# Optimization experiments

Hardware: AMD Instinct MI355X
Metric: run time of the kernel (lower is better)

Reference implementation:

```python
import jax, jax.numpy as jnp
import numpy as np

ALPHA = 0.2  # LeakyReLU negative slope
NEG_INF = -9e15


def gat_layer(h_in, adj_mask, W, a, concat):
    """Classic pyGAT dense GraphAttentionLayer (eval mode, dropout=identity).
    h_in: [B, N, Fin], adj_mask: [N, N] bool, W: [Fin, Fout], a: [2*Fout, 1].
    """
    h = jnp.einsum('bnf,fo->bno', h_in, W)          # [B, N, Fout]
    Fo = W.shape[1]
    f1 = h @ a[:Fo, 0]                               # [B, N] scores for source
    f2 = h @ a[Fo:, 0]                               # [B, N] scores for target
    e = jax.nn.leaky_relu(f1[:, :, None] + f2[:, None, :], negative_slope=ALPHA)
    e = jnp.where(adj_mask[None, :, :], e, NEG_INF)  # mask non-edges
    attn = jax.nn.softmax(e, axis=-1)                # normalize over neighbors
    out = jnp.einsum('bij,bjo->bio', attn, h)        # weighted aggregation
    return jax.nn.elu(out) if concat else out


def setup_inputs() -> dict:
    key = jax.random.key(0)
    ks = jax.random.split(key, 7)
    B, T, N = 2, 17, 1024
    nfeat, nhid, nclass, nheads = 64, 64, 64, 4
    x = jax.random.normal(ks[0], (B, T, N, nfeat), dtype=jnp.float32)
    adj = jax.random.randint(ks[1], (N, N), 0, 2, dtype=jnp.int32)
    W_heads = jax.random.normal(ks[2], (nheads, nfeat, nhid), dtype=jnp.float32) / np.sqrt(nfeat)
    a_heads = jax.random.normal(ks[3], (nheads, 2 * nhid, 1), dtype=jnp.float32) / np.sqrt(2 * nhid)
    W_out = jax.random.normal(ks[4], (nhid * nheads, nclass), dtype=jnp.float32) / np.sqrt(nhid * nheads)
    a_out = jax.random.normal(ks[5], (2 * nclass, 1), dtype=jnp.float32) / np.sqrt(2 * nclass)
    return {"x": x, "adj": adj, "W_heads": W_heads, "a_heads": a_heads,
            "W_out": W_out, "a_out": a_out, "pred_step": 1}


def reference(x, adj, W_heads, a_heads, W_out, a_out, pred_step):
    B, T, N, F = x.shape
    Tp = T - pred_step
    mask = adj > 0
    # All time steps are independent -> fold (B, Tp) into one batch axis.
    xt = x[:, :Tp].reshape(B * Tp, N, F)
    nheads = W_heads.shape[0]
    heads = [gat_layer(xt, mask, W_heads[h], a_heads[h], concat=True)
             for h in range(nheads)]
    hcat = jnp.concatenate(heads, axis=-1)           # [B*Tp, N, nhid*nheads]
    out = jax.nn.relu(gat_layer(hcat, mask, W_out, a_out, concat=False))
    return out.reshape(B, Tp, N, -1)
```

## Files before the change

kernel.cpp:

```cpp
#include <hip/hip_runtime.h>
#include <hip/hip_bf16.h>

typedef short bf16x8 __attribute__((ext_vector_type(8)));
typedef float f32x4 __attribute__((ext_vector_type(4)));
typedef _Float16 half8 __attribute__((ext_vector_type(8)));
typedef _Float16 half4 __attribute__((ext_vector_type(4)));
typedef __fp16 cvt2_t __attribute__((ext_vector_type(2)));

#define N_NODES 1024
#define FDIM 64
#define NG 32
#define LOG2E 1.44269504088896f

__global__ __launch_bounds__(256) void k_maskf(const int* __restrict__ adj,
                                               __hip_bfloat16* __restrict__ Madd) {
    int w = blockIdx.x * 256 + threadIdx.x;
    const int* p = adj + (size_t)w * 32;
    union { bf16x8 v[4]; __hip_bfloat16 hh[32]; } u;
#pragma unroll
    for (int b = 0; b < 32; b++)
        u.hh[b] = __float2bfloat16(p[b] > 0 ? 0.f : -2048.f);
    bf16x8* dst = (bf16x8*)(Madd + (size_t)w * 32);
#pragma unroll
    for (int q = 0; q < 4; q++) dst[q] = u.v[q];
}

__global__ __launch_bounds__(256) void k_prepw(const float* __restrict__ Wh,
                                               const float* __restrict__ Wo,
                                               _Float16* __restrict__ wt1,
                                               _Float16* __restrict__ wt2) {
    const int t = threadIdx.x;
    {
        const int h = t >> 6, o = t & 63;
        const float* src = Wh + (size_t)h * 4096 + o;
#pragma unroll
        for (int k0 = 0; k0 < 64; k0 += 8) {
            union { half8 v; cvt2_t c[4]; } pk_;
#pragma unroll
            for (int kk = 0; kk < 8; kk += 2)
                pk_.c[kk >> 1] = __builtin_amdgcn_cvt_pkrtz(src[(k0 + kk) * 64],
                                                            src[(k0 + kk + 1) * 64]);
            *(half8*)(wt1 + (size_t)t * 64 + k0) = pk_.v;
        }
    }
    {
        const int kq = t >> 6, o = t & 63;
        const float* src = Wo + o;
#pragma unroll
        for (int k0 = kq * 64; k0 < kq * 64 + 64; k0 += 8) {
            union { half8 v; cvt2_t c[4]; } pk_;
#pragma unroll
            for (int kk = 0; kk < 8; kk += 2)
                pk_.c[kk >> 1] = __builtin_amdgcn_cvt_pkrtz(src[(k0 + kk) * 64],
                                                            src[(k0 + kk + 1) * 64]);
            *(half8*)(wt2 + (size_t)o * 256 + k0) = pk_.v;
        }
    }
}

__global__ __launch_bounds__(512, 2) void k_proj1(const float* __restrict__ x,
                                                  const _Float16* __restrict__ wt1,
                                                  const float* __restrict__ ah,
                                                  _Float16* __restrict__ H1T,
                                                  float* __restrict__ F1,
                                                  float* __restrict__ F2) {
    __shared__ _Float16 xs[128][64];
    const int t = threadIdx.x;
    const int nb = blockIdx.x, g = blockIdx.y;
    const int n0 = nb * 128;
    const int b = g >> 4, tstep = g & 15;

    {
        const int r = t >> 2, cq = t & 3;
        const float* xr = x + (((size_t)(b * 17 + tstep) * N_NODES + n0 + r) * FDIM) + cq * 16;
        float4 v0 = *(const float4*)(xr);
        float4 v1 = *(const float4*)(xr + 4);
        float4 v2 = *(const float4*)(xr + 8);
        float4 v3 = *(const float4*)(xr + 12);
        union { half8 v; cvt2_t c[4]; } u0, u1;
        u0.c[0] = __builtin_amdgcn_cvt_pkrtz(v0.x, v0.y);
        u0.c[1] = __builtin_amdgcn_cvt_pkrtz(v0.z, v0.w);
        u0.c[2] = __builtin_amdgcn_cvt_pkrtz(v1.x, v1.y);
        u0.c[3] = __builtin_amdgcn_cvt_pkrtz(v1.z, v1.w);
        u1.c[0] = __builtin_amdgcn_cvt_pkrtz(v2.x, v2.y);
        u1.c[1] = __builtin_amdgcn_cvt_pkrtz(v2.z, v2.w);
        u1.c[2] = __builtin_amdgcn_cvt_pkrtz(v3.x, v3.y);
        u1.c[3] = __builtin_amdgcn_cvt_pkrtz(v3.z, v3.w);
        *(half8*)&xs[r][((2 * cq) ^ (r & 7)) * 8] = u0.v;
        *(half8*)&xs[r][((2 * cq + 1) ^ (r & 7)) * 8] = u1.v;
    }
    __syncthreads();

    const int wv = t >> 6, ln = t & 63, li = ln & 15, grp = ln >> 4;
    const int arow = wv * 16 + li;

    f32x4 acc[16];
#pragma unroll
    for (int q = 0; q < 16; q++) acc[q] = (f32x4){0.f, 0.f, 0.f, 0.f};

#pragma unroll
    for (int s = 0; s < 2; s++) {
        half8 af = *(const half8*)&xs[arow][((s * 4 + grp) ^ (arow & 7)) * 8];
#pragma unroll
        for (int tile = 0; tile < 16; tile++) {
            half8 bf = *(const half8*)(wt1 + (size_t)(tile * 16 + li) * 64 + s * 32 + grp * 8);
            acc[tile] = __builtin_amdgcn_mfma_f32_16x16x32_f16(af, bf, acc[tile], 0, 0, 0);
        }
    }

    const int nbase = n0 + wv * 16 + grp * 4;
#pragma unroll
    for (int h = 0; h < 4; h++) {
        float p1[4] = {0.f, 0.f, 0.f, 0.f}, p2[4] = {0.f, 0.f, 0.f, 0.f};
#pragma unroll
        for (int ot = 0; ot < 4; ot++) {
            float a1v = ah[h * 128 + ot * 16 + li];
            float a2v = ah[h * 128 + 64 + ot * 16 + li];
            f32x4 A = acc[h * 4 + ot];
#pragma unroll
            for (int r = 0; r < 4; r++) {
                p1[r] = fmaf(A[r], a1v, p1[r]);
                p2[r] = fmaf(A[r], a2v, p2[r]);
            }
        }
#pragma unroll
        for (int m = 1; m < 16; m <<= 1)
#pragma unroll
            for (int r = 0; r < 4; r++) {
                p1[r] += __shfl_xor(p1[r], m);
                p2[r] += __shfl_xor(p2[r], m);
            }
        if (li == 0) {
            const size_t gh = (size_t)h * NG + g;
#pragma unroll
            for (int r = 0; r < 4; r++) {
                F1[gh * N_NODES + nbase + r] = p1[r] * LOG2E;
                F2[gh * N_NODES + nbase + r] = p2[r] * LOG2E;
            }
        }
    }
#pragma unroll
    for (int tile = 0; tile < 16; tile++) {
        const int h = tile >> 2, ot = tile & 3;
        union { half4 v; cvt2_t c[2]; } st;
        st.c[0] = __builtin_amdgcn_cvt_pkrtz(acc[tile][0], acc[tile][1]);
        st.c[1] = __builtin_amdgcn_cvt_pkrtz(acc[tile][2], acc[tile][3]);
        _Float16* dst = H1T + (((size_t)h * NG + g) * FDIM + ot * 16 + li) * N_NODES + nbase;
        *(half4*)dst = st.v;
    }
}

template<int CONCAT>
__global__ __launch_bounds__(512, 4) void k_attn(
    const _Float16* __restrict__ HT,
    const float* __restrict__ F1,
    const float* __restrict__ F2,
    const __hip_bfloat16* __restrict__ Madd,
    _Float16* __restrict__ HC,
    float* __restrict__ out)
{
    __shared__ _Float16 vt[64][256];
    __shared__ float f2s[N_NODES];
    const int t = threadIdx.x;
    const int g = blockIdx.x, h = blockIdx.y, nb = blockIdx.z;
    const int i0 = nb * 128;
    const size_t gidx = CONCAT ? ((size_t)h * NG + g) : (size_t)g;

    ((float2*)f2s)[t] = ((const float2*)(F2 + gidx * N_NODES))[t];

    const int wv = t >> 6, ln = t & 63;
    const int li = ln & 15, grp = ln >> 4, jb = grp * 8;
    const int lx = li & 7;
    const int il = wv * 16 + li;
    const float f1v = F1[gidx * N_NODES + i0 + il];

    const _Float16* Hg = HT + gidx * (size_t)(FDIM * N_NODES);
    const int srow = wv * 8 + (ln >> 3);
    const int swu = (ln & 7) ^ (srow & 7);
    const _Float16* srcb = Hg + (size_t)srow * N_NODES + (ln & 7) * 8;
    const __hip_bfloat16* Mp = Madd + (size_t)(i0 + il) * N_NODES + jb;

    f32x4 acc[4], acc5;
#pragma unroll
    for (int q = 0; q < 4; q++) acc[q] = (f32x4){0.f, 0.f, 0.f, 0.f};
    acc5 = (f32x4){0.f, 0.f, 0.f, 0.f};

    union { half8 v; unsigned short s[8]; } onesu;
#pragma unroll
    for (int q = 0; q < 8; q++) onesu.s[q] = 0x3C00;
    const half8 ones = onesu.v;

    half8 stg[4];
#pragma unroll
    for (int k2 = 0; k2 < 4; k2++) stg[k2] = *(const half8*)(srcb + k2 * 64);
    bf16x8 m0 = *(const bf16x8*)Mp;
    bf16x8 m1 = *(const bf16x8*)(Mp + 32);

    for (int jt = 0; jt < 4; jt++) {
        __syncthreads();
#pragma unroll
        for (int k2 = 0; k2 < 4; k2++)
            *(half8*)&vt[srow][(k2 * 8 + swu) * 8] = stg[k2];
        if (jt < 3) {
#pragma unroll
            for (int k2 = 0; k2 < 4; k2++)
                stg[k2] = *(const half8*)(srcb + (jt + 1) * 256 + k2 * 64);
        }
        __syncthreads();

#pragma unroll
        for (int jc = 0; jc < 8; jc++) {
            union { bf16x8 v; unsigned u[4]; } mc;
            mc.v = m0;
            m0 = m1;
            if (!(jt == 3 && jc >= 6))
                m1 = *(const bf16x8*)(Mp + 64);
            Mp += 32;

            const float* f2p = &f2s[jt * 256 + jc * 32 + jb];
            float4 fa = *(const float4*)f2p;
            float4 fb = *(const float4*)(f2p + 4);
            union { half8 v; cvt2_t c[4]; } afr;
            {
                float mlo, mhi, s0, s1;
                mlo = __uint_as_float(mc.u[0] << 16);
                mhi = __uint_as_float(mc.u[0] & 0xffff0000u);
                s0 = f1v + fa.x + mlo; s1 = f1v + fa.y + mhi;
                s0 = fmaxf(s0, 0.2f * s0); s1 = fmaxf(s1, 0.2f * s1);
                afr.c[0] = __builtin_amdgcn_cvt_pkrtz(__builtin_amdgcn_exp2f(s0),
                                                      __builtin_amdgcn_exp2f(s1));
                mlo = __uint_as_float(mc.u[1] << 16);
                mhi = __uint_as_float(mc.u[1] & 0xffff0000u);
                s0 = f1v + fa.z + mlo; s1 = f1v + fa.w + mhi;
                s0 = fmaxf(s0, 0.2f * s0); s1 = fmaxf(s1, 0.2f * s1);
                afr.c[1] = __builtin_amdgcn_cvt_pkrtz(__builtin_amdgcn_exp2f(s0),
                                                      __builtin_amdgcn_exp2f(s1));
                mlo = __uint_as_float(mc.u[2] << 16);
                mhi = __uint_as_float(mc.u[2] & 0xffff0000u);
                s0 = f1v + fb.x + mlo; s1 = f1v + fb.y + mhi;
                s0 = fmaxf(s0, 0.2f * s0); s1 = fmaxf(s1, 0.2f * s1);
                afr.c[2] = __builtin_amdgcn_cvt_pkrtz(__builtin_amdgcn_exp2f(s0),
                                                      __builtin_amdgcn_exp2f(s1));
                mlo = __uint_as_float(mc.u[3] << 16);
                mhi = __uint_as_float(mc.u[3] & 0xffff0000u);
                s0 = f1v + fb.z + mlo; s1 = f1v + fb.w + mhi;
                s0 = fmaxf(s0, 0.2f * s0); s1 = fmaxf(s1, 0.2f * s1);
                afr.c[3] = __builtin_amdgcn_cvt_pkrtz(__builtin_amdgcn_exp2f(s0),
                                                      __builtin_amdgcn_exp2f(s1));
            }
            const int ub = (jc >> 1) * 8 + (((jc & 1) * 4 + grp) ^ lx);
#pragma unroll
            for (int q = 0; q < 4; q++) {
                half8 bfr = *(const half8*)&vt[q * 16 + li][ub * 8];
                acc[q] = __builtin_amdgcn_mfma_f32_16x16x32_f16(afr.v, bfr, acc[q], 0, 0, 0);
            }
            acc5 = __builtin_amdgcn_mfma_f32_16x16x32_f16(afr.v, ones, acc5, 0, 0, 0);
        }
    }

    float rin[4];
#pragma unroll
    for (int r2 = 0; r2 < 4; r2++) rin[r2] = 1.0f / acc5[r2];

    if (CONCAT) {
        _Float16* HCg = HC + (size_t)g * N_NODES * 256 + h * 64;
#pragma unroll
        for (int q = 0; q < 4; q++)
#pragma unroll
            for (int r2 = 0; r2 < 4; r2++) {
                int irow = wv * 16 + grp * 4 + r2;
                float v = acc[q][r2] * rin[r2];
                v = v > 0.f ? v : expm1f(v);
                HCg[(size_t)(i0 + irow) * 256 + q * 16 + li] = (_Float16)v;
            }
    } else {
        float* og = out + (size_t)g * N_NODES * FDIM;
#pragma unroll
        for (int q = 0; q < 4; q++)
#pragma unroll
            for (int r2 = 0; r2 < 4; r2++) {
                int irow = wv * 16 + grp * 4 + r2;
                float v = acc[q][r2] * rin[r2];
                og[(size_t)(i0 + irow) * FDIM + q * 16 + li] = v > 0.f ? v : 0.f;
            }
    }
}

__global__ __launch_bounds__(512, 2) void k_proj2(const _Float16* __restrict__ HC,
                                                  const _Float16* __restrict__ wt2,
                                                  const float* __restrict__ ao,
                                                  _Float16* __restrict__ H2T,
                                                  float* __restrict__ F1b,
                                                  float* __restrict__ F2b) {
    __shared__ _Float16 xs[128][256];
    const int t = threadIdx.x;
    const int nb = blockIdx.x, g = blockIdx.y;
    const int n0 = nb * 128;

    {
        const int r = t >> 2, cq = t & 3;
        const _Float16* src = HC + ((size_t)g * N_NODES + n0 + r) * 256 + cq * 64;
#pragma unroll
        for (int uu = 0; uu < 8; uu++) {
            int u = cq * 8 + uu;
            half8 v = *(const half8*)(src + uu * 8);
            int us = (u & 24) | ((u ^ r) & 7);
            *(half8*)&xs[r][us * 8] = v;
        }
    }
    __syncthreads();

    const int wv = t >> 6, ln = t & 63, li = ln & 15, grp = ln >> 4;
    const int arow = wv * 16 + li;

    f32x4 acc[4];
#pragma unroll
    for (int q = 0; q < 4; q++) acc[q] = (f32x4){0.f, 0.f, 0.f, 0.f};

#pragma unroll
    for (int s = 0; s < 8; s++) {
        int u = s * 4 + grp;
        int us = (u & 24) | ((u ^ arow) & 7);
        half8 af = *(const half8*)&xs[arow][us * 8];
#pragma unroll
        for (int tile = 0; tile < 4; tile++) {
            half8 bf = *(const half8*)(wt2 + (size_t)(tile * 16 + li) * 256 + s * 32 + grp * 8);
            acc[tile] = __builtin_amdgcn_mfma_f32_16x16x32_f16(af, bf, acc[tile], 0, 0, 0);
        }
    }

    const int nbase = n0 + wv * 16 + grp * 4;
    {
        float p1[4] = {0.f, 0.f, 0.f, 0.f}, p2[4] = {0.f, 0.f, 0.f, 0.f};
#pragma unroll
        for (int ot = 0; ot < 4; ot++) {
            float a1v = ao[ot * 16 + li];
            float a2v = ao[64 + ot * 16 + li];
            f32x4 A = acc[ot];
#pragma unroll
            for (int r = 0; r < 4; r++) {
                p1[r] = fmaf(A[r], a1v, p1[r]);
                p2[r] = fmaf(A[r], a2v, p2[r]);
            }
        }
#pragma unroll
        for (int m = 1; m < 16; m <<= 1)
#pragma unroll
            for (int r = 0; r < 4; r++) {
                p1[r] += __shfl_xor(p1[r], m);
                p2[r] += __shfl_xor(p2[r], m);
            }
        if (li == 0) {
#pragma unroll
            for (int r = 0; r < 4; r++) {
                F1b[(size_t)g * N_NODES + nbase + r] = p1[r] * LOG2E;
                F2b[(size_t)g * N_NODES + nbase + r] = p2[r] * LOG2E;
            }
        }
    }
#pragma unroll
    for (int tile = 0; tile < 4; tile++) {
        union { half4 v; cvt2_t c[2]; } st;
        st.c[0] = __builtin_amdgcn_cvt_pkrtz(acc[tile][0], acc[tile][1]);
        st.c[1] = __builtin_amdgcn_cvt_pkrtz(acc[tile][2], acc[tile][3]);
        _Float16* dst = H2T + ((size_t)g * FDIM + tile * 16 + li) * N_NODES + nbase;
        *(half4*)dst = st.v;
    }
}

extern "C" void kernel_launch(void* const* d_in, const int* in_sizes, int n_in,
                              void* d_out, int out_size, void* d_ws, size_t ws_size,
                              hipStream_t stream) {
    const float* x  = (const float*)d_in[0];
    const int* adj  = (const int*)d_in[1];
    const float* Wh = (const float*)d_in[2];
    const float* ah = (const float*)d_in[3];
    const float* Wo = (const float*)d_in[4];
    const float* ao = (const float*)d_in[5];

    char* ws = (char*)d_ws;
    __hip_bfloat16* Madd = (__hip_bfloat16*)(ws);
    _Float16* wt1 = (_Float16*)(ws + 2097152);
    _Float16* wt2 = (_Float16*)(ws + 2129920);
    float* F1  = (float*)(ws + 2162688);
    float* F2  = (float*)(ws + 2686976);
    float* F1b = (float*)(ws + 3211264);
    float* F2b = (float*)(ws + 3342336);
    _Float16* H1T = (_Float16*)(ws + 3473408);
    _Float16* HC  = (_Float16*)(ws + 3473408 + 16777216);
    _Float16* H2T = (_Float16*)(ws + 3473408 + 33554432);
    float* out = (float*)d_out;

    k_maskf  <<<dim3(128),       dim3(256), 0, stream>>>(adj, Madd);
    k_prepw  <<<dim3(1),         dim3(256), 0, stream>>>(Wh, Wo, wt1, wt2);
    k_proj1  <<<dim3(8, 32),     dim3(512), 0, stream>>>(x, wt1, ah, H1T, F1, F2);
    k_attn<1><<<dim3(32, 4, 8),  dim3(512), 0, stream>>>(H1T, F1, F2, Madd, HC, nullptr);
    k_proj2  <<<dim3(8, 32),     dim3(512), 0, stream>>>(HC, wt2, ao, H2T, F1b, F2b);
    k_attn<0><<<dim3(32, 1, 8),  dim3(512), 0, stream>>>(H2T, F1b, F2b, Madd, nullptr, out);
}
```

Baseline: 113.6 us.

## Double-buffer attention V tiles and merge mask/weight prep kernels

The attention kernel now keeps two shared-memory V tiles, so the next tile is written while the current one feeds the MFMAs, and only one barrier per tile remains instead of two. Global prefetch runs two tiles ahead. The mask conversion and weight conversion kernels are merged into one launch, and the weight transpose is spread over 8 blocks instead of one. The trade-off is doubled LDS use (about 68KB per block), which can reduce occupancy below the launch-bounds target of 4 blocks per CU.

```diff
diff --git a/kernel.cpp b/kernel.cpp
--- a/kernel.cpp
+++ b/kernel.cpp
@@ -12,48 +12,49 @@
 #define NG 32
 #define LOG2E 1.44269504088896f
 
-__global__ __launch_bounds__(256) void k_maskf(const int* __restrict__ adj,
-                                               __hip_bfloat16* __restrict__ Madd) {
-    int w = blockIdx.x * 256 + threadIdx.x;
-    const int* p = adj + (size_t)w * 32;
-    union { bf16x8 v[4]; __hip_bfloat16 hh[32]; } u;
-#pragma unroll
-    for (int b = 0; b < 32; b++)
-        u.hh[b] = __float2bfloat16(p[b] > 0 ? 0.f : -2048.f);
-    bf16x8* dst = (bf16x8*)(Madd + (size_t)w * 32);
-#pragma unroll
-    for (int q = 0; q < 4; q++) dst[q] = u.v[q];
-}
-
-__global__ __launch_bounds__(256) void k_prepw(const float* __restrict__ Wh,
-                                               const float* __restrict__ Wo,
-                                               _Float16* __restrict__ wt1,
-                                               _Float16* __restrict__ wt2) {
-    const int t = threadIdx.x;
-    {
-        const int h = t >> 6, o = t & 63;
-        const float* src = Wh + (size_t)h * 4096 + o;
-#pragma unroll
-        for (int k0 = 0; k0 < 64; k0 += 8) {
+__global__ __launch_bounds__(256) void k_prep(const int* __restrict__ adj,
+                                              const float* __restrict__ Wh,
+                                              const float* __restrict__ Wo,
+                                              __hip_bfloat16* __restrict__ Madd,
+                                              _Float16* __restrict__ wt1,
+                                              _Float16* __restrict__ wt2) {
+    const int bb = blockIdx.x, t = threadIdx.x;
+    if (bb < 128) {
+        int w = bb * 256 + t;
+        const int* p = adj + (size_t)w * 32;
+        union { bf16x8 v[4]; __hip_bfloat16 hh[32]; } u;
+#pragma unroll
+        for (int b = 0; b < 32; b++)
+            u.hh[b] = __float2bfloat16(p[b] > 0 ? 0.f : -2048.f);
+        bf16x8* dst = (bf16x8*)(Madd + (size_t)w * 32);
+#pragma unroll
+        for (int q = 0; q < 4; q++) dst[q] = u.v[q];
+    } else if (bb < 132) {
+        const int row = (bb - 128) * 64 + (t >> 2);
+        const int kq = t & 3;
+        const float* src = Wh + (size_t)(row >> 6) * 4096 + (row & 63);
+#pragma unroll
+        for (int kk = 0; kk < 16; kk += 8) {
+            const int k0 = kq * 16 + kk;
             union { half8 v; cvt2_t c[4]; } pk_;
 #pragma unroll
-            for (int kk = 0; kk < 8; kk += 2)
-                pk_.c[kk >> 1] = __builtin_amdgcn_cvt_pkrtz(src[(k0 + kk) * 64],
-                                                            src[(k0 + kk + 1) * 64]);
-            *(half8*)(wt1 + (size_t)t * 64 + k0) = pk_.v;
-        }
-    }
-    {
-        const int kq = t >> 6, o = t & 63;
+            for (int j = 0; j < 8; j += 2)
+                pk_.c[j >> 1] = __builtin_amdgcn_cvt_pkrtz(src[(k0 + j) * 64],
+                                                           src[(k0 + j + 1) * 64]);
+            *(half8*)(wt1 + (size_t)row * 64 + k0) = pk_.v;
+        }
+    } else {
+        const int o = (bb - 132) * 16 + (t >> 4);
+        const int k0 = (t & 15) * 16;
         const float* src = Wo + o;
 #pragma unroll
-        for (int k0 = kq * 64; k0 < kq * 64 + 64; k0 += 8) {
+        for (int kk = 0; kk < 16; kk += 8) {
             union { half8 v; cvt2_t c[4]; } pk_;
 #pragma unroll
-            for (int kk = 0; kk < 8; kk += 2)
-                pk_.c[kk >> 1] = __builtin_amdgcn_cvt_pkrtz(src[(k0 + kk) * 64],
-                                                            src[(k0 + kk + 1) * 64]);
-            *(half8*)(wt2 + (size_t)o * 256 + k0) = pk_.v;
+            for (int j = 0; j < 8; j += 2)
+                pk_.c[j >> 1] = __builtin_amdgcn_cvt_pkrtz(src[(k0 + kk + j) * 64],
+                                                           src[(k0 + kk + j + 1) * 64]);
+            *(half8*)(wt2 + (size_t)o * 256 + k0 + kk) = pk_.v;
         }
     }
 }
@@ -159,7 +160,7 @@
     _Float16* __restrict__ HC,
     float* __restrict__ out)
 {
-    __shared__ _Float16 vt[64][256];
+    __shared__ _Float16 vt[2][64][256];
     __shared__ float f2s[N_NODES];
     const int t = threadIdx.x;
     const int g = blockIdx.x, h = blockIdx.y, nb = blockIdx.z;
@@ -193,20 +194,26 @@
     half8 stg[4];
 #pragma unroll
     for (int k2 = 0; k2 < 4; k2++) stg[k2] = *(const half8*)(srcb + k2 * 64);
+#pragma unroll
+    for (int k2 = 0; k2 < 4; k2++)
+        *(half8*)&vt[0][srow][(k2 * 8 + swu) * 8] = stg[k2];
+#pragma unroll
+    for (int k2 = 0; k2 < 4; k2++) stg[k2] = *(const half8*)(srcb + 256 + k2 * 64);
     bf16x8 m0 = *(const bf16x8*)Mp;
     bf16x8 m1 = *(const bf16x8*)(Mp + 32);
+    __syncthreads();
 
     for (int jt = 0; jt < 4; jt++) {
-        __syncthreads();
-#pragma unroll
-        for (int k2 = 0; k2 < 4; k2++)
-            *(half8*)&vt[srow][(k2 * 8 + swu) * 8] = stg[k2];
         if (jt < 3) {
 #pragma unroll
             for (int k2 = 0; k2 < 4; k2++)
-                stg[k2] = *(const half8*)(srcb + (jt + 1) * 256 + k2 * 64);
-        }
-        __syncthreads();
+                *(half8*)&vt[(jt + 1) & 1][srow][(k2 * 8 + swu) * 8] = stg[k2];
+        }
+        if (jt < 2) {
+#pragma unroll
+            for (int k2 = 0; k2 < 4; k2++)
+                stg[k2] = *(const half8*)(srcb + (jt + 2) * 256 + k2 * 64);
+        }
 
 #pragma unroll
         for (int jc = 0; jc < 8; jc++) {
@@ -251,11 +258,12 @@
             const int ub = (jc >> 1) * 8 + (((jc & 1) * 4 + grp) ^ lx);
 #pragma unroll
             for (int q = 0; q < 4; q++) {
-                half8 bfr = *(const half8*)&vt[q * 16 + li][ub * 8];
+                half8 bfr = *(const half8*)&vt[jt & 1][q * 16 + li][ub * 8];
                 acc[q] = __builtin_amdgcn_mfma_f32_16x16x32_f16(afr.v, bfr, acc[q], 0, 0, 0);
             }
             acc5 = __builtin_amdgcn_mfma_f32_16x16x32_f16(afr.v, ones, acc5, 0, 0, 0);
         }
+        if (jt < 3) __syncthreads();
     }
 
     float rin[4];
@@ -391,8 +399,7 @@
     _Float16* H2T = (_Float16*)(ws + 3473408 + 33554432);
     float* out = (float*)d_out;
 
-    k_maskf  <<<dim3(128),       dim3(256), 0, stream>>>(adj, Madd);
-    k_prepw  <<<dim3(1),         dim3(256), 0, stream>>>(Wh, Wo, wt1, wt2);
+    k_prep   <<<dim3(136),       dim3(256), 0, stream>>>(adj, Wh, Wo, Madd, wt1, wt2);
     k_proj1  <<<dim3(8, 32),     dim3(512), 0, stream>>>(x, wt1, ah, H1T, F1, F2);
     k_attn<1><<<dim3(32, 4, 8),  dim3(512), 0, stream>>>(H1T, F1, F2, Madd, HC, nullptr);
     k_proj2  <<<dim3(8, 32),     dim3(512), 0, stream>>>(HC, wt2, ao, H2T, F1b, F2b);
```

Result: faster. 111.3 us (-2.0%).
